# Performance work log

Hardware: AMD Instinct MI355X
Metric: run time of the kernel (lower is better)

The kernel has to match this reference:

```python
import jax, jax.numpy as jnp
import numpy as np

GAMMA = 0.7
WALK_LEN = 3
TAU = 1.0
N_FILTERS = 8


def _row_norm(A):
    return A / jnp.clip(jnp.sum(A, axis=-1, keepdims=True), 1e-12, None)


def _motif_channel(A, idx, Wadj, gates):
    # A: [n,n]; idx: [I,k] int node indices; Wadj: [F,k,k]; gates: [L]
    n = A.shape[0]
    I, k = idx.shape
    F = Wadj.shape[0]
    # learnable filter adjacency: softplus, symmetrize, zero diagonal, row-normalize
    S = jax.nn.softplus(Wadj)
    S = 0.5 * (S + jnp.swapaxes(S, -1, -2)) * (1.0 - jnp.eye(k, dtype=A.dtype))
    Sf = _row_norm(S)                                  # [F,k,k]
    # per-instance induced subgraph transition matrices
    As = A[idx[:, :, None], idx[:, None, :]]           # [I,k,k]
    Tm = _row_norm(As)                                 # [I,k,k]
    # batched Kronecker product: Km[i,f,a*k+b,c*k+d] = Tm[i,a,c]*Sf[f,b,d]
    Km = (Tm[:, None, :, None, :, None] * Sf[None, :, None, :, None, :]).reshape(I, F, k * k, k * k)
    gp = jax.nn.softplus(gates)                        # [L] length gates
    M = Km
    acc = (GAMMA * gp[0]) * jnp.trace(M, axis1=-2, axis2=-1)   # [I,F]
    for p in range(2, WALK_LEN + 1):
        M = M @ Km
        acc = acc + (GAMMA ** p * gp[p - 1]) * jnp.trace(M, axis1=-2, axis2=-1)
    sims = acc                                         # [I,F] RWK similarities
    alphas = jax.nn.softmax(sims / max(1e-06, TAU), axis=-1)
    contrib = (alphas * sims) / float(k)               # [I,F]
    upd = jnp.broadcast_to(contrib[:, None, :], (I, k, F)).reshape(I * k, F)
    return jnp.zeros((n, F), A.dtype).at[idx.reshape(-1)].add(upd)


def _layer(A, tri_idx, cyc_idx, H, Wt, Wc, g, lng, lnb, w1, b1, w2, b2):
    Phi = jnp.concatenate([_motif_channel(A, tri_idx, Wt, g),
                           _motif_channel(A, cyc_idx, Wc, g),
                           H], axis=1)                 # [n, in_ch]
    mu = jnp.mean(Phi, axis=-1, keepdims=True)
    var = jnp.var(Phi, axis=-1, keepdims=True)
    X = (Phi - mu) / jnp.sqrt(var + 1e-5) * lng + lnb  # LayerNorm
    return jax.nn.gelu(X @ w1 + b1, approximate=False) @ w2 + b2  # dropout = identity (eval)


def _templates():
    tri = np.zeros((3, 3), np.float32)
    for u, v in [(0, 1), (1, 2), (0, 2)]:
        tri[u, v] = tri[v, u] = 1.0
    cyc = np.zeros((4, 4), np.float32)
    for u, v in [(0, 1), (1, 2), (2, 3), (3, 0)]:
        cyc[u, v] = cyc[v, u] = 1.0
    return tri, cyc


def setup_inputs() -> dict:
    key = jax.random.key(0)
    ks = jax.random.split(key, 16)
    n, D, HID = 4096, 128, 128
    A = (jax.random.uniform(ks[0], (n, n)) < 0.01).astype(jnp.float32)
    A = 0.5 * (A + A.T)
    A = A * (1.0 - jnp.eye(n, dtype=jnp.float32))
    tri_idx = jax.random.randint(ks[1], (30000, 3), 0, n, dtype=jnp.int32)
    cyc_idx = jax.random.randint(ks[2], (15000, 4), 0, n, dtype=jnp.int32)
    tri_t, cyc_t = _templates()
    def w_adj(k, tmpl):
        return jnp.asarray(tmpl)[None] + 0.05 * jax.random.normal(k, (N_FILTERS,) + tmpl.shape, dtype=jnp.float32)
    in0, in1 = 17, 145
    inp = {"A_full": A, "tri_idx": tri_idx, "cyc_idx": cyc_idx,
           "W_tri_0": w_adj(ks[3], tri_t), "W_cyc_0": w_adj(ks[4], cyc_t),
           "gates_0": jnp.zeros((WALK_LEN,), jnp.float32),
           "lng_0": jnp.ones((in0,), jnp.float32), "lnb_0": jnp.zeros((in0,), jnp.float32),
           "w1_0": 0.05 * jax.random.normal(ks[5], (in0, HID), jnp.float32), "b1_0": jnp.zeros((HID,), jnp.float32),
           "w2_0": 0.05 * jax.random.normal(ks[6], (HID, D), jnp.float32), "b2_0": jnp.zeros((D,), jnp.float32),
           "W_tri_1": w_adj(ks[7], tri_t), "W_cyc_1": w_adj(ks[8], cyc_t),
           "gates_1": jnp.zeros((WALK_LEN,), jnp.float32),
           "lng_1": jnp.ones((in1,), jnp.float32), "lnb_1": jnp.zeros((in1,), jnp.float32),
           "w1_1": 0.05 * jax.random.normal(ks[9], (in1, HID), jnp.float32), "b1_1": jnp.zeros((HID,), jnp.float32),
           "w2_1": 0.05 * jax.random.normal(ks[10], (HID, D), jnp.float32), "b2_1": jnp.zeros((D,), jnp.float32)}
    return inp


def reference(A_full, tri_idx, cyc_idx,
              W_tri_0, W_cyc_0, gates_0, lng_0, lnb_0, w1_0, b1_0, w2_0, b2_0,
              W_tri_1, W_cyc_1, gates_1, lng_1, lnb_1, w1_1, b1_1, w2_1, b2_1):
    # base channel (use_base=True): node degree from dense adjacency
    H = jnp.sum(A_full, axis=-1, keepdims=True)        # [n,1]
    Z = _layer(A_full, tri_idx, cyc_idx, H, W_tri_0, W_cyc_0, gates_0, lng_0, lnb_0, w1_0, b1_0, w2_0, b2_0)
    H = jnp.concatenate([Z, H], axis=1)                # residual_cat: [n,129]
    Z = _layer(A_full, tri_idx, cyc_idx, H, W_tri_1, W_cyc_1, gates_1, lng_1, lnb_1, w1_1, b1_1, w2_1, b2_1)
    H = jnp.concatenate([Z, H], axis=1)                # [n,257]
    return H
```

## Files before the change

kernel.cpp:

```cpp
#include <hip/hip_runtime.h>
#include <math.h>
#include <stdint.h>

#define GAMMA 0.7f
#define QCAP 4608
#define NT 1024

typedef __attribute__((ext_vector_type(8))) short short8v;
typedef __attribute__((ext_vector_type(4))) float f32x4;

__device__ __forceinline__ float sp_dev(float x) {
    return fmaxf(x, 0.0f) + log1pf(expf(-fabsf(x)));
}
__device__ __forceinline__ float gelu_exact(float x) {
    return 0.5f * x * (1.0f + erff(x * 0.70710678118654752f));
}
__device__ __forceinline__ uint16_t f2bf(float x) {
    union { float f; uint32_t u; } c; c.f = x;
    uint32_t u = c.u + 0x7FFFu + ((c.u >> 16) & 1u);
    return (uint16_t)(u >> 16);
}

__device__ __forceinline__ short8v wfrag(const float* __restrict__ W, int col,
                                         int k0, int kmax) {
    short8v r;
#pragma unroll
    for (int j = 0; j < 8; j++) {
        int k = k0 + j;
        float v = (k < kmax) ? W[(size_t)k * 128 + col] : 0.0f;
        r[j] = (short)f2bf(v);
    }
    return r;
}

__global__ __launch_bounds__(NT) void uber_kernel(
    const float* __restrict__ A, const int* __restrict__ tri, const int* __restrict__ cyc,
    const float* __restrict__ Wt0, const float* __restrict__ Wc0, const float* __restrict__ g0,
    const float* __restrict__ lng0, const float* __restrict__ lnb0,
    const float* __restrict__ w1_0, const float* __restrict__ b1_0,
    const float* __restrict__ w2_0, const float* __restrict__ b2_0,
    const float* __restrict__ Wt1, const float* __restrict__ Wc1, const float* __restrict__ g1,
    const float* __restrict__ lng1, const float* __restrict__ lnb1,
    const float* __restrict__ w1_1, const float* __restrict__ b1_1,
    const float* __restrict__ w2_1, const float* __restrict__ b2_1,
    float* __restrict__ out, int n, int Itri, int Icyc) {

    __shared__ __align__(16) char upool[QCAP * 4];
    int* queue = (int*)upool;
    uint16_t (*Xs)[168] = (uint16_t(*)[168])upool;
    uint16_t (*Hs)[136] = (uint16_t(*)[136])(upool + 5376);
    float    (*Zs)[132] = (float(*)[132])(upool + 9728);
    __shared__ float dcs[2][2][8][3];
    __shared__ float phiL0[16][16];
    __shared__ float phiL1[16][16];
    __shared__ float h0s[16];
    __shared__ int qcnt;

    const int tid  = threadIdx.x;
    const int v0   = blockIdx.x * 16;
    const int wave = tid >> 6;
    const int lane = tid & 63;

    if (tid < 256) { ((float*)phiL0)[tid] = 0.0f; ((float*)phiL1)[tid] = 0.0f; }
    if (tid == 0) qcnt = 0;
    if (tid < 32) {
        int L = tid >> 4, m = (tid >> 3) & 1, f = tid & 7;
        int k = m ? 4 : 3;
        const float* W = L ? (m ? Wc1 : Wt1) : (m ? Wc0 : Wt0);
        const float* g = L ? g1 : g0;
        float S[4][4], Y[4][4];
        for (int a = 0; a < k; a++)
            for (int b = 0; b < k; b++)
                S[a][b] = sp_dev(W[(f * k + a) * k + b]);
        for (int a = 0; a < k; a++)
            for (int b = 0; b < k; b++)
                Y[a][b] = (a == b) ? 0.0f : 0.5f * (S[a][b] + S[b][a]);
        for (int a = 0; a < k; a++) {
            float rs = 0.0f;
            for (int b = 0; b < k; b++) rs += Y[a][b];
            rs = fmaxf(rs, 1e-12f);
            for (int b = 0; b < k; b++) Y[a][b] /= rs;
        }
        float t1 = 0, t2 = 0, t3 = 0;
        for (int a = 0; a < k; a++) t1 += Y[a][a];
        for (int a = 0; a < k; a++)
            for (int b = 0; b < k; b++) t2 += Y[a][b] * Y[b][a];
        for (int a = 0; a < k; a++)
            for (int b = 0; b < k; b++)
                for (int c = 0; c < k; c++) t3 += Y[a][b] * Y[b][c] * Y[c][a];
        dcs[m][L][f][0] = GAMMA * sp_dev(g[0]) * t1;
        dcs[m][L][f][1] = GAMMA * GAMMA * sp_dev(g[1]) * t2;
        dcs[m][L][f][2] = GAMMA * GAMMA * GAMMA * sp_dev(g[2]) * t3;
    }

    {
        int rr = wave;
        const float4* Ar = (const float4*)(A + (size_t)(v0 + rr) * n);
        int n4 = n >> 2;
        float s0 = 0, s1 = 0, s2 = 0, s3 = 0;
        for (int i = lane; i < n4; i += 256) {
            float4 a = Ar[i], b = Ar[i + 64], c = Ar[i + 128], d = Ar[i + 192];
            s0 += a.x + a.y + a.z + a.w;
            s1 += b.x + b.y + b.z + b.w;
            s2 += c.x + c.y + c.z + c.w;
            s3 += d.x + d.y + d.z + d.w;
        }
        float s = (s0 + s1) + (s2 + s3);
        for (int o = 32; o > 0; o >>= 1) s += __shfl_down(s, o);
        if (lane == 0) {
            h0s[rr] = s;
            out[(size_t)(v0 + rr) * 257 + 256] = s;
        }
    }
    __syncthreads();

    {
        int tot = Itri + Icyc;
        for (int base = 0; base < tot; base += NT) {
            int inst = base + tid;
            if (inst >= tot) break;
            int hit = 0;
            if (inst < Itri) {
                const int* p = tri + inst * 3;
#pragma unroll
                for (int j = 0; j < 3; j++) hit |= ((unsigned)(p[j] - v0) < 16u);
            } else {
                const int* p = cyc + (size_t)(inst - Itri) * 4;
#pragma unroll
                for (int j = 0; j < 4; j++) hit |= ((unsigned)(p[j] - v0) < 16u);
            }
            if (hit) {
                int q = atomicAdd(&qcnt, 1);
                if (q < QCAP) queue[q] = inst;
            }
        }
    }
    __syncthreads();

    {
        int qn = qcnt < QCAP ? qcnt : QCAP;
        for (int qi = tid; qi < qn; qi += NT) {
            int inst = queue[qi];
            bool isTri = inst < Itri;
            int m = isTri ? 0 : 1;
            float kinv = isTri ? (1.0f / 3.0f) : 0.25f;
            int nd[4];
            if (isTri) {
                const int* p = tri + inst * 3;
                nd[0] = p[0]; nd[1] = p[1]; nd[2] = p[2]; nd[3] = 0;
            } else {
                const int* p = cyc + (size_t)(inst - Itri) * 4;
                nd[0] = p[0]; nd[1] = p[1]; nd[2] = p[2]; nd[3] = p[3];
            }
            float M[4][4];
#pragma unroll
            for (int a = 0; a < 4; a++) {
                float rs = 0.0f;
#pragma unroll
                for (int b = 0; b < 4; b++) {
                    float v;
                    if (isTri)
                        v = (a < 3 && b < 3) ? A[(size_t)nd[a] * n + nd[b]]
                                             : ((a == 3 && b == 3) ? 1.0f : 0.0f);
                    else
                        v = A[(size_t)nd[a] * n + nd[b]];
                    M[a][b] = v; rs += v;
                }
                rs = fmaxf(rs, 1e-12f);
                float inv = 1.0f / rs;
#pragma unroll
                for (int b = 0; b < 4; b++) M[a][b] *= inv;
            }
            float t1 = M[0][0] + M[1][1] + M[2][2] + M[3][3];
            float t2 = 0, t3 = 0;
#pragma unroll
            for (int a = 0; a < 4; a++)
#pragma unroll
                for (int b = 0; b < 4; b++) {
                    float ab = M[a][b];
                    t2 += ab * M[b][a];
                    float a3 = 0;
#pragma unroll
                    for (int c = 0; c < 4; c++) a3 += M[b][c] * M[c][a];
                    t3 += ab * a3;
                }
            if (isTri) { t1 -= 1.0f; t2 -= 1.0f; t3 -= 1.0f; }

            float cn[2][8];
#pragma unroll
            for (int L = 0; L < 2; L++) {
                float sims[8], mx = -1e30f;
#pragma unroll
                for (int f = 0; f < 8; f++) {
                    sims[f] = dcs[m][L][f][0] * t1 + dcs[m][L][f][1] * t2 +
                              dcs[m][L][f][2] * t3;
                    mx = fmaxf(mx, sims[f]);
                }
                float se = 0;
#pragma unroll
                for (int f = 0; f < 8; f++) { float e = expf(sims[f] - mx); cn[L][f] = e; se += e; }
                float si = 1.0f / se;
#pragma unroll
                for (int f = 0; f < 8; f++) cn[L][f] = cn[L][f] * si * sims[f] * kinv;
            }
            int K = isTri ? 3 : 4;
#pragma unroll
            for (int j = 0; j < 4; j++) {
                if (j >= K) break;
                int r = nd[j] - v0;
                if ((unsigned)r < 16u) {
#pragma unroll
                    for (int f = 0; f < 8; f++) {
                        atomicAdd(&phiL0[r][m * 8 + f], cn[0][f]);
                        atomicAdd(&phiL1[r][m * 8 + f], cn[1][f]);
                    }
                }
            }
        }
    }
    __syncthreads();

    if (tid < 512) {
        int r = tid >> 5;
        int j = tid & 31;
        float x = (j < 16) ? phiL0[r][j] : (j == 16 ? h0s[r] : 0.0f);
        float s1 = x, s2 = x * x;
        for (int o = 16; o > 0; o >>= 1) { s1 += __shfl_xor(s1, o); s2 += __shfl_xor(s2, o); }
        float mu = s1 / 17.0f;
        float rstd = rsqrtf(s2 / 17.0f - mu * mu + 1e-5f);
        Xs[r][j] = (j < 17) ? f2bf((x - mu) * rstd * lng0[j] + lnb0[j]) : (uint16_t)0;
    }
    __syncthreads();

    if (tid < 512) {
        int w8 = tid >> 6, lr = lane & 15, lg = lane >> 4;
        int col = w8 * 16 + lr;
        f32x4 acc = {0.f, 0.f, 0.f, 0.f};
        short8v a = *(const short8v*)&Xs[lr][lg * 8];
        short8v b = wfrag(w1_0, col, lg * 8, 17);
        acc = __builtin_amdgcn_mfma_f32_16x16x32_bf16(a, b, acc, 0, 0, 0);
        float bias = b1_0[col];
#pragma unroll
        for (int i = 0; i < 4; i++)
            Hs[lg * 4 + i][col] = f2bf(gelu_exact(acc[i] + bias));
    }
    __syncthreads();

    if (tid < 512) {
        int w8 = tid >> 6, lr = lane & 15, lg = lane >> 4;
        int col = w8 * 16 + lr;
        f32x4 acc = {0.f, 0.f, 0.f, 0.f};
#pragma unroll
        for (int ks = 0; ks < 4; ks++) {
            short8v a = *(const short8v*)&Hs[lr][ks * 32 + lg * 8];
            short8v b = wfrag(w2_0, col, ks * 32 + lg * 8, 128);
            acc = __builtin_amdgcn_mfma_f32_16x16x32_bf16(a, b, acc, 0, 0, 0);
        }
        float bias = b2_0[col];
#pragma unroll
        for (int i = 0; i < 4; i++) {
            int row = lg * 4 + i;
            float val = acc[i] + bias;
            out[(size_t)(v0 + row) * 257 + 128 + col] = val;
            Zs[row][col] = val;
        }
    }
    __syncthreads();

    if (tid < 512) {
        int rr = tid >> 5;
        int t = tid & 31;
        float ph[5];
        float s1 = 0.0f, s2 = 0.0f;
#pragma unroll
        for (int s = 0; s < 5; s++) {
            int j = t + 32 * s;
            float x = 0.0f;
            if (j < 16) x = phiL1[rr][j];
            else if (j < 144) x = Zs[rr][j - 16];
            else if (j == 144) x = h0s[rr];
            ph[s] = x;
            if (j < 145) { s1 += x; s2 += x * x; }
        }
        for (int o = 16; o > 0; o >>= 1) { s1 += __shfl_xor(s1, o); s2 += __shfl_xor(s2, o); }
        float mu = s1 / 145.0f;
        float rstd = rsqrtf(s2 / 145.0f - mu * mu + 1e-5f);
#pragma unroll
        for (int s = 0; s < 5; s++) {
            int j = t + 32 * s;
            Xs[rr][j] = (j < 145) ? f2bf((ph[s] - mu) * rstd * lng1[j] + lnb1[j])
                                  : (uint16_t)0;
        }
    }
    __syncthreads();

    if (tid < 512) {
        int w8 = tid >> 6, lr = lane & 15, lg = lane >> 4;
        int col = w8 * 16 + lr;
        f32x4 acc = {0.f, 0.f, 0.f, 0.f};
#pragma unroll
        for (int ks = 0; ks < 5; ks++) {
            short8v a = *(const short8v*)&Xs[lr][ks * 32 + lg * 8];
            short8v b = wfrag(w1_1, col, ks * 32 + lg * 8, 145);
            acc = __builtin_amdgcn_mfma_f32_16x16x32_bf16(a, b, acc, 0, 0, 0);
        }
        float bias = b1_1[col];
#pragma unroll
        for (int i = 0; i < 4; i++)
            Hs[lg * 4 + i][col] = f2bf(gelu_exact(acc[i] + bias));
    }
    __syncthreads();

    if (tid < 512) {
        int w8 = tid >> 6, lr = lane & 15, lg = lane >> 4;
        int col = w8 * 16 + lr;
        f32x4 acc = {0.f, 0.f, 0.f, 0.f};
#pragma unroll
        for (int ks = 0; ks < 4; ks++) {
            short8v a = *(const short8v*)&Hs[lr][ks * 32 + lg * 8];
            short8v b = wfrag(w2_1, col, ks * 32 + lg * 8, 128);
            acc = __builtin_amdgcn_mfma_f32_16x16x32_bf16(a, b, acc, 0, 0, 0);
        }
        float bias = b2_1[col];
#pragma unroll
        for (int i = 0; i < 4; i++) {
            int row = lg * 4 + i;
            out[(size_t)(v0 + row) * 257 + col] = acc[i] + bias;
        }
    }
}

extern "C" void kernel_launch(void* const* d_in, const int* in_sizes, int n_in,
                              void* d_out, int out_size, void* d_ws, size_t ws_size,
                              hipStream_t stream) {
    const float* A    = (const float*)d_in[0];
    const int*   tri  = (const int*)d_in[1];
    const int*   cyc  = (const int*)d_in[2];

    int n    = out_size / 257;
    int Itri = in_sizes[1] / 3;
    int Icyc = in_sizes[2] / 4;

    uber_kernel<<<n / 16, NT, 0, stream>>>(
        A, tri, cyc,
        (const float*)d_in[3], (const float*)d_in[4], (const float*)d_in[5],
        (const float*)d_in[6], (const float*)d_in[7],
        (const float*)d_in[8], (const float*)d_in[9],
        (const float*)d_in[10], (const float*)d_in[11],
        (const float*)d_in[12], (const float*)d_in[13], (const float*)d_in[14],
        (const float*)d_in[15], (const float*)d_in[16],
        (const float*)d_in[17], (const float*)d_in[18],
        (const float*)d_in[19], (const float*)d_in[20],
        (float*)d_out, n, Itri, Icyc);
}
```

Measured before the change: 90.93 us.

## Split fused kernel into per-instance motif pass and per-node MLP pass

Adds a first kernel that computes each motif instance's softmax-weighted contribution exactly once, together with degree row sums and pre-packed bf16 transposed weight matrices written to workspace. The second kernel then only scans and scatters those precomputed contributions and loads the packed weight fragments directly. Previously each 16-node block recomputed the induced-subgraph traces for every instance it touched and converted fp32 weights to bf16 inline. The split removes that redundant per-block work but adds a second launch and workspace round trips, and the smaller QCAP could overflow on denser graphs.

```diff
diff --git a/kernel.cpp b/kernel.cpp
--- a/kernel.cpp
+++ b/kernel.cpp
@@ -3,8 +3,7 @@
 #include <stdint.h>
 
 #define GAMMA 0.7f
-#define QCAP 4608
-#define NT 1024
+#define QCAP 2048
 
 typedef __attribute__((ext_vector_type(8))) short short8v;
 typedef __attribute__((ext_vector_type(4))) float f32x4;
@@ -21,199 +20,235 @@
     return (uint16_t)(u >> 16);
 }
 
-__device__ __forceinline__ short8v wfrag(const float* __restrict__ W, int col,
-                                         int k0, int kmax) {
-    short8v r;
-#pragma unroll
-    for (int j = 0; j < 8; j++) {
-        int k = k0 + j;
-        float v = (k < kmax) ? W[(size_t)k * 128 + col] : 0.0f;
-        r[j] = (short)f2bf(v);
-    }
-    return r;
-}
-
-__global__ __launch_bounds__(NT) void uber_kernel(
+__global__ __launch_bounds__(256) void k1_kernel(
     const float* __restrict__ A, const int* __restrict__ tri, const int* __restrict__ cyc,
     const float* __restrict__ Wt0, const float* __restrict__ Wc0, const float* __restrict__ g0,
+    const float* __restrict__ Wt1, const float* __restrict__ Wc1, const float* __restrict__ g1,
+    const float* __restrict__ w1_0, const float* __restrict__ w2_0,
+    const float* __restrict__ w1_1, const float* __restrict__ w2_1,
+    float* __restrict__ cont, float* __restrict__ H0,
+    uint16_t* __restrict__ Wb10, uint16_t* __restrict__ Wb20,
+    uint16_t* __restrict__ Wb11, uint16_t* __restrict__ Wb21,
+    float* __restrict__ out, int n, int Itri, int Icyc, int BC) {
+
+    const int tid = threadIdx.x;
+    const int bid = blockIdx.x;
+    const int Itot = Itri + Icyc;
+
+    if (bid < BC) {
+        __shared__ float dcs[2][2][8][3];
+        if (tid < 32) {
+            int L = tid >> 4, m = (tid >> 3) & 1, f = tid & 7;
+            int k = m ? 4 : 3;
+            const float* W = L ? (m ? Wc1 : Wt1) : (m ? Wc0 : Wt0);
+            const float* g = L ? g1 : g0;
+            float S[4][4], Y[4][4];
+            for (int a = 0; a < k; a++)
+                for (int b = 0; b < k; b++)
+                    S[a][b] = sp_dev(W[(f * k + a) * k + b]);
+            for (int a = 0; a < k; a++)
+                for (int b = 0; b < k; b++)
+                    Y[a][b] = (a == b) ? 0.0f : 0.5f * (S[a][b] + S[b][a]);
+            for (int a = 0; a < k; a++) {
+                float rs = 0.0f;
+                for (int b = 0; b < k; b++) rs += Y[a][b];
+                rs = fmaxf(rs, 1e-12f);
+                for (int b = 0; b < k; b++) Y[a][b] /= rs;
+            }
+            float t1 = 0, t2 = 0, t3 = 0;
+            for (int a = 0; a < k; a++) t1 += Y[a][a];
+            for (int a = 0; a < k; a++)
+                for (int b = 0; b < k; b++) t2 += Y[a][b] * Y[b][a];
+            for (int a = 0; a < k; a++)
+                for (int b = 0; b < k; b++)
+                    for (int c = 0; c < k; c++) t3 += Y[a][b] * Y[b][c] * Y[c][a];
+            dcs[m][L][f][0] = GAMMA * sp_dev(g[0]) * t1;
+            dcs[m][L][f][1] = GAMMA * GAMMA * sp_dev(g[1]) * t2;
+            dcs[m][L][f][2] = GAMMA * GAMMA * GAMMA * sp_dev(g[2]) * t3;
+        }
+        __syncthreads();
+
+        int inst = bid * 256 + tid;
+        if (inst >= Itot) return;
+        bool isTri = inst < Itri;
+        int m = isTri ? 0 : 1;
+        float kinv = isTri ? (1.0f / 3.0f) : 0.25f;
+        int nd[4];
+        if (isTri) {
+            const int* p = tri + inst * 3;
+            nd[0] = p[0]; nd[1] = p[1]; nd[2] = p[2]; nd[3] = 0;
+        } else {
+            const int* p = cyc + (size_t)(inst - Itri) * 4;
+            nd[0] = p[0]; nd[1] = p[1]; nd[2] = p[2]; nd[3] = p[3];
+        }
+        float M[4][4];
+#pragma unroll
+        for (int a = 0; a < 4; a++) {
+            float rs = 0.0f;
+#pragma unroll
+            for (int b = 0; b < 4; b++) {
+                float v;
+                if (isTri)
+                    v = (a < 3 && b < 3) ? A[(size_t)nd[a] * n + nd[b]]
+                                         : ((a == 3 && b == 3) ? 1.0f : 0.0f);
+                else
+                    v = A[(size_t)nd[a] * n + nd[b]];
+                M[a][b] = v; rs += v;
+            }
+            rs = fmaxf(rs, 1e-12f);
+            float inv = 1.0f / rs;
+#pragma unroll
+            for (int b = 0; b < 4; b++) M[a][b] *= inv;
+        }
+        float t1 = M[0][0] + M[1][1] + M[2][2] + M[3][3];
+        float t2 = 0, t3 = 0;
+#pragma unroll
+        for (int a = 0; a < 4; a++)
+#pragma unroll
+            for (int b = 0; b < 4; b++) {
+                float ab = M[a][b];
+                t2 += ab * M[b][a];
+                float a3 = 0;
+#pragma unroll
+                for (int c = 0; c < 4; c++) a3 += M[b][c] * M[c][a];
+                t3 += ab * a3;
+            }
+        if (isTri) { t1 -= 1.0f; t2 -= 1.0f; t3 -= 1.0f; }
+
+#pragma unroll
+        for (int L = 0; L < 2; L++) {
+            float sims[8], mx = -1e30f;
+#pragma unroll
+            for (int f = 0; f < 8; f++) {
+                sims[f] = dcs[m][L][f][0] * t1 + dcs[m][L][f][1] * t2 +
+                          dcs[m][L][f][2] * t3;
+                mx = fmaxf(mx, sims[f]);
+            }
+            float es[8], se = 0;
+#pragma unroll
+            for (int f = 0; f < 8; f++) { es[f] = expf(sims[f] - mx); se += es[f]; }
+            float si = 1.0f / se;
+            f32x4 c0, c1;
+#pragma unroll
+            for (int f = 0; f < 4; f++) c0[f] = es[f] * si * sims[f] * kinv;
+#pragma unroll
+            for (int f = 0; f < 4; f++) c1[f] = es[f + 4] * si * sims[f + 4] * kinv;
+            float* cp = cont + ((size_t)L * Itot + inst) * 8;
+            *(f32x4*)cp = c0;
+            *(f32x4*)(cp + 4) = c1;
+        }
+    } else if (bid < BC + n) {
+        __shared__ float red[4];
+        int row = bid - BC;
+        const float4* Arow = (const float4*)(A + (size_t)row * n);
+        int n4 = n >> 2;
+        float s = 0.0f;
+        for (int i = tid; i < n4; i += 256) {
+            float4 v = Arow[i];
+            s += v.x + v.y + v.z + v.w;
+        }
+        for (int off = 32; off > 0; off >>= 1) s += __shfl_down(s, off);
+        if ((tid & 63) == 0) red[tid >> 6] = s;
+        __syncthreads();
+        if (tid == 0) {
+            float t = red[0] + red[1] + red[2] + red[3];
+            H0[row] = t;
+            out[(size_t)row * 257 + 256] = t;
+        }
+    } else {
+        int base = (bid - BC - n) * 4096;
+        for (int k = 0; k < 16; k++) {
+            int idx = base + k * 256 + tid;
+            if (idx >= 57344) break;
+            if (idx < 4096) {
+                int c = idx >> 5, kk = idx & 31;
+                Wb10[idx] = (kk < 17) ? f2bf(w1_0[kk * 128 + c]) : 0;
+            } else if (idx < 20480) {
+                int e = idx - 4096; int c = e >> 7, kk = e & 127;
+                Wb20[e] = f2bf(w2_0[kk * 128 + c]);
+            } else if (idx < 40960) {
+                int e = idx - 20480; int c = e / 160, kk = e % 160;
+                Wb11[e] = (kk < 145) ? f2bf(w1_1[kk * 128 + c]) : 0;
+            } else {
+                int e = idx - 40960; int c = e >> 7, kk = e & 127;
+                Wb21[e] = f2bf(w2_1[kk * 128 + c]);
+            }
+        }
+    }
+}
+
+__global__ __launch_bounds__(1024) void k2_kernel(
+    const int* __restrict__ tri, const int* __restrict__ cyc,
+    const float* __restrict__ cont, const float* __restrict__ H0,
     const float* __restrict__ lng0, const float* __restrict__ lnb0,
-    const float* __restrict__ w1_0, const float* __restrict__ b1_0,
-    const float* __restrict__ w2_0, const float* __restrict__ b2_0,
-    const float* __restrict__ Wt1, const float* __restrict__ Wc1, const float* __restrict__ g1,
+    const uint16_t* __restrict__ Wb10, const float* __restrict__ b1_0,
+    const uint16_t* __restrict__ Wb20, const float* __restrict__ b2_0,
     const float* __restrict__ lng1, const float* __restrict__ lnb1,
-    const float* __restrict__ w1_1, const float* __restrict__ b1_1,
-    const float* __restrict__ w2_1, const float* __restrict__ b2_1,
+    const uint16_t* __restrict__ Wb11, const float* __restrict__ b1_1,
+    const uint16_t* __restrict__ Wb21, const float* __restrict__ b2_1,
     float* __restrict__ out, int n, int Itri, int Icyc) {
 
-    __shared__ __align__(16) char upool[QCAP * 4];
+    __shared__ __align__(16) char upool[18432];
     int* queue = (int*)upool;
     uint16_t (*Xs)[168] = (uint16_t(*)[168])upool;
     uint16_t (*Hs)[136] = (uint16_t(*)[136])(upool + 5376);
     float    (*Zs)[132] = (float(*)[132])(upool + 9728);
-    __shared__ float dcs[2][2][8][3];
-    __shared__ float phiL0[16][16];
-    __shared__ float phiL1[16][16];
+    __shared__ float phi[2][16][16];
     __shared__ float h0s[16];
     __shared__ int qcnt;
 
     const int tid  = threadIdx.x;
     const int v0   = blockIdx.x * 16;
-    const int wave = tid >> 6;
     const int lane = tid & 63;
-
-    if (tid < 256) { ((float*)phiL0)[tid] = 0.0f; ((float*)phiL1)[tid] = 0.0f; }
+    const int Itot = Itri + Icyc;
+
+    if (tid < 512) ((float*)phi)[tid] = 0.0f;
     if (tid == 0) qcnt = 0;
-    if (tid < 32) {
-        int L = tid >> 4, m = (tid >> 3) & 1, f = tid & 7;
-        int k = m ? 4 : 3;
-        const float* W = L ? (m ? Wc1 : Wt1) : (m ? Wc0 : Wt0);
-        const float* g = L ? g1 : g0;
-        float S[4][4], Y[4][4];
-        for (int a = 0; a < k; a++)
-            for (int b = 0; b < k; b++)
-                S[a][b] = sp_dev(W[(f * k + a) * k + b]);
-        for (int a = 0; a < k; a++)
-            for (int b = 0; b < k; b++)
-                Y[a][b] = (a == b) ? 0.0f : 0.5f * (S[a][b] + S[b][a]);
-        for (int a = 0; a < k; a++) {
-            float rs = 0.0f;
-            for (int b = 0; b < k; b++) rs += Y[a][b];
-            rs = fmaxf(rs, 1e-12f);
-            for (int b = 0; b < k; b++) Y[a][b] /= rs;
-        }
-        float t1 = 0, t2 = 0, t3 = 0;
-        for (int a = 0; a < k; a++) t1 += Y[a][a];
-        for (int a = 0; a < k; a++)
-            for (int b = 0; b < k; b++) t2 += Y[a][b] * Y[b][a];
-        for (int a = 0; a < k; a++)
-            for (int b = 0; b < k; b++)
-                for (int c = 0; c < k; c++) t3 += Y[a][b] * Y[b][c] * Y[c][a];
-        dcs[m][L][f][0] = GAMMA * sp_dev(g[0]) * t1;
-        dcs[m][L][f][1] = GAMMA * GAMMA * sp_dev(g[1]) * t2;
-        dcs[m][L][f][2] = GAMMA * GAMMA * GAMMA * sp_dev(g[2]) * t3;
-    }
-
-    {
-        int rr = wave;
-        const float4* Ar = (const float4*)(A + (size_t)(v0 + rr) * n);
-        int n4 = n >> 2;
-        float s0 = 0, s1 = 0, s2 = 0, s3 = 0;
-        for (int i = lane; i < n4; i += 256) {
-            float4 a = Ar[i], b = Ar[i + 64], c = Ar[i + 128], d = Ar[i + 192];
-            s0 += a.x + a.y + a.z + a.w;
-            s1 += b.x + b.y + b.z + b.w;
-            s2 += c.x + c.y + c.z + c.w;
-            s3 += d.x + d.y + d.z + d.w;
-        }
-        float s = (s0 + s1) + (s2 + s3);
-        for (int o = 32; o > 0; o >>= 1) s += __shfl_down(s, o);
-        if (lane == 0) {
-            h0s[rr] = s;
-            out[(size_t)(v0 + rr) * 257 + 256] = s;
-        }
-    }
-    __syncthreads();
-
-    {
-        int tot = Itri + Icyc;
-        for (int base = 0; base < tot; base += NT) {
-            int inst = base + tid;
-            if (inst >= tot) break;
-            int hit = 0;
-            if (inst < Itri) {
-                const int* p = tri + inst * 3;
-#pragma unroll
-                for (int j = 0; j < 3; j++) hit |= ((unsigned)(p[j] - v0) < 16u);
-            } else {
-                const int* p = cyc + (size_t)(inst - Itri) * 4;
-#pragma unroll
-                for (int j = 0; j < 4; j++) hit |= ((unsigned)(p[j] - v0) < 16u);
-            }
-            if (hit) {
-                int q = atomicAdd(&qcnt, 1);
-                if (q < QCAP) queue[q] = inst;
-            }
+    if (tid >= 512 && tid < 528) h0s[tid - 512] = H0[v0 + (tid - 512)];
+    __syncthreads();
+
+    for (int base = 0; base < Itot; base += 1024) {
+        int inst = base + tid;
+        if (inst >= Itot) break;
+        int hit = 0;
+        if (inst < Itri) {
+            const int* p = tri + inst * 3;
+#pragma unroll
+            for (int j = 0; j < 3; j++) hit |= ((unsigned)(p[j] - v0) < 16u);
+        } else {
+            const int* p = cyc + (size_t)(inst - Itri) * 4;
+#pragma unroll
+            for (int j = 0; j < 4; j++) hit |= ((unsigned)(p[j] - v0) < 16u);
+        }
+        if (hit) {
+            int q = atomicAdd(&qcnt, 1);
+            if (q < QCAP) queue[q] = inst;
         }
     }
     __syncthreads();
 
     {
         int qn = qcnt < QCAP ? qcnt : QCAP;
-        for (int qi = tid; qi < qn; qi += NT) {
+        for (int it = tid; it < 2 * qn; it += 1024) {
+            int qi = it >> 1, L = it & 1;
             int inst = queue[qi];
             bool isTri = inst < Itri;
+            int K = isTri ? 3 : 4;
             int m = isTri ? 0 : 1;
-            float kinv = isTri ? (1.0f / 3.0f) : 0.25f;
-            int nd[4];
-            if (isTri) {
-                const int* p = tri + inst * 3;
-                nd[0] = p[0]; nd[1] = p[1]; nd[2] = p[2]; nd[3] = 0;
-            } else {
-                const int* p = cyc + (size_t)(inst - Itri) * 4;
-                nd[0] = p[0]; nd[1] = p[1]; nd[2] = p[2]; nd[3] = p[3];
-            }
-            float M[4][4];
-#pragma unroll
-            for (int a = 0; a < 4; a++) {
-                float rs = 0.0f;
-#pragma unroll
-                for (int b = 0; b < 4; b++) {
-                    float v;
-                    if (isTri)
-                        v = (a < 3 && b < 3) ? A[(size_t)nd[a] * n + nd[b]]
-                                             : ((a == 3 && b == 3) ? 1.0f : 0.0f);
-                    else
-                        v = A[(size_t)nd[a] * n + nd[b]];
-                    M[a][b] = v; rs += v;
-                }
-                rs = fmaxf(rs, 1e-12f);
-                float inv = 1.0f / rs;
-#pragma unroll
-                for (int b = 0; b < 4; b++) M[a][b] *= inv;
-            }
-            float t1 = M[0][0] + M[1][1] + M[2][2] + M[3][3];
-            float t2 = 0, t3 = 0;
-#pragma unroll
-            for (int a = 0; a < 4; a++)
-#pragma unroll
-                for (int b = 0; b < 4; b++) {
-                    float ab = M[a][b];
-                    t2 += ab * M[b][a];
-                    float a3 = 0;
-#pragma unroll
-                    for (int c = 0; c < 4; c++) a3 += M[b][c] * M[c][a];
-                    t3 += ab * a3;
-                }
-            if (isTri) { t1 -= 1.0f; t2 -= 1.0f; t3 -= 1.0f; }
-
-            float cn[2][8];
-#pragma unroll
-            for (int L = 0; L < 2; L++) {
-                float sims[8], mx = -1e30f;
-#pragma unroll
-                for (int f = 0; f < 8; f++) {
-                    sims[f] = dcs[m][L][f][0] * t1 + dcs[m][L][f][1] * t2 +
-                              dcs[m][L][f][2] * t3;
-                    mx = fmaxf(mx, sims[f]);
-                }
-                float se = 0;
-#pragma unroll
-                for (int f = 0; f < 8; f++) { float e = expf(sims[f] - mx); cn[L][f] = e; se += e; }
-                float si = 1.0f / se;
-#pragma unroll
-                for (int f = 0; f < 8; f++) cn[L][f] = cn[L][f] * si * sims[f] * kinv;
-            }
-            int K = isTri ? 3 : 4;
+            const int* p = isTri ? tri + inst * 3 : cyc + (size_t)(inst - Itri) * 4;
+            const float* cp = cont + ((size_t)L * Itot + inst) * 8;
+            float4 c0 = *(const float4*)cp;
+            float4 c1 = *(const float4*)(cp + 4);
 #pragma unroll
             for (int j = 0; j < 4; j++) {
                 if (j >= K) break;
-                int r = nd[j] - v0;
+                int r = p[j] - v0;
                 if ((unsigned)r < 16u) {
-#pragma unroll
-                    for (int f = 0; f < 8; f++) {
-                        atomicAdd(&phiL0[r][m * 8 + f], cn[0][f]);
-                        atomicAdd(&phiL1[r][m * 8 + f], cn[1][f]);
-                    }
+                    float* dst = &phi[L][r][m * 8];
+                    atomicAdd(&dst[0], c0.x); atomicAdd(&dst[1], c0.y);
+                    atomicAdd(&dst[2], c0.z); atomicAdd(&dst[3], c0.w);
+                    atomicAdd(&dst[4], c1.x); atomicAdd(&dst[5], c1.y);
+                    atomicAdd(&dst[6], c1.z); atomicAdd(&dst[7], c1.w);
                 }
             }
         }
@@ -223,7 +258,7 @@
     if (tid < 512) {
         int r = tid >> 5;
         int j = tid & 31;
-        float x = (j < 16) ? phiL0[r][j] : (j == 16 ? h0s[r] : 0.0f);
+        float x = (j < 16) ? phi[0][r][j] : (j == 16 ? h0s[r] : 0.0f);
         float s1 = x, s2 = x * x;
         for (int o = 16; o > 0; o >>= 1) { s1 += __shfl_xor(s1, o); s2 += __shfl_xor(s2, o); }
         float mu = s1 / 17.0f;
@@ -237,7 +272,7 @@
         int col = w8 * 16 + lr;
         f32x4 acc = {0.f, 0.f, 0.f, 0.f};
         short8v a = *(const short8v*)&Xs[lr][lg * 8];
-        short8v b = wfrag(w1_0, col, lg * 8, 17);
+        short8v b = *(const short8v*)(Wb10 + (size_t)col * 32 + lg * 8);
         acc = __builtin_amdgcn_mfma_f32_16x16x32_bf16(a, b, acc, 0, 0, 0);
         float bias = b1_0[col];
 #pragma unroll
@@ -253,7 +288,7 @@
 #pragma unroll
         for (int ks = 0; ks < 4; ks++) {
             short8v a = *(const short8v*)&Hs[lr][ks * 32 + lg * 8];
-            short8v b = wfrag(w2_0, col, ks * 32 + lg * 8, 128);
+            short8v b = *(const short8v*)(Wb20 + (size_t)col * 128 + ks * 32 + lg * 8);
             acc = __builtin_amdgcn_mfma_f32_16x16x32_bf16(a, b, acc, 0, 0, 0);
         }
         float bias = b2_0[col];
@@ -276,7 +311,7 @@
         for (int s = 0; s < 5; s++) {
             int j = t + 32 * s;
             float x = 0.0f;
-            if (j < 16) x = phiL1[rr][j];
+            if (j < 16) x = phi[1][rr][j];
             else if (j < 144) x = Zs[rr][j - 16];
             else if (j == 144) x = h0s[rr];
             ph[s] = x;
@@ -301,7 +336,7 @@
 #pragma unroll
         for (int ks = 0; ks < 5; ks++) {
             short8v a = *(const short8v*)&Xs[lr][ks * 32 + lg * 8];
-            short8v b = wfrag(w1_1, col, ks * 32 + lg * 8, 145);
+            short8v b = *(const short8v*)(Wb11 + (size_t)col * 160 + ks * 32 + lg * 8);
             acc = __builtin_amdgcn_mfma_f32_16x16x32_bf16(a, b, acc, 0, 0, 0);
         }
         float bias = b1_1[col];
@@ -318,7 +353,7 @@
 #pragma unroll
         for (int ks = 0; ks < 4; ks++) {
             short8v a = *(const short8v*)&Hs[lr][ks * 32 + lg * 8];
-            short8v b = wfrag(w2_1, col, ks * 32 + lg * 8, 128);
+            short8v b = *(const short8v*)(Wb21 + (size_t)col * 128 + ks * 32 + lg * 8);
             acc = __builtin_amdgcn_mfma_f32_16x16x32_bf16(a, b, acc, 0, 0, 0);
         }
         float bias = b2_1[col];
@@ -340,16 +375,32 @@
     int n    = out_size / 257;
     int Itri = in_sizes[1] / 3;
     int Icyc = in_sizes[2] / 4;
-
-    uber_kernel<<<n / 16, NT, 0, stream>>>(
+    int Itot = Itri + Icyc;
+
+    float* ws = (float*)d_ws;
+    float* H0   = ws;
+    float* cont = ws + n;
+    uint16_t* Wb10 = (uint16_t*)(cont + (size_t)2 * Itot * 8);
+    uint16_t* Wb20 = Wb10 + 128 * 32;
+    uint16_t* Wb11 = Wb20 + 128 * 128;
+    uint16_t* Wb21 = Wb11 + 128 * 160;
+    float* out = (float*)d_out;
+
+    int BC = (Itot + 255) / 256;
+    int BP = 14;
+    k1_kernel<<<BC + n + BP, 256, 0, stream>>>(
         A, tri, cyc,
         (const float*)d_in[3], (const float*)d_in[4], (const float*)d_in[5],
+        (const float*)d_in[12], (const float*)d_in[13], (const float*)d_in[14],
+        (const float*)d_in[8], (const float*)d_in[10],
+        (const float*)d_in[17], (const float*)d_in[19],
+        cont, H0, Wb10, Wb20, Wb11, Wb21, out, n, Itri, Icyc, BC);
+
+    k2_kernel<<<n / 16, 1024, 0, stream>>>(
+        tri, cyc, cont, H0,
         (const float*)d_in[6], (const float*)d_in[7],
-        (const float*)d_in[8], (const float*)d_in[9],
-        (const float*)d_in[10], (const float*)d_in[11],
-        (const float*)d_in[12], (const float*)d_in[13], (const float*)d_in[14],
+        Wb10, (const float*)d_in[9], Wb20, (const float*)d_in[11],
         (const float*)d_in[15], (const float*)d_in[16],
-        (const float*)d_in[17], (const float*)d_in[18],
-        (const float*)d_in[19], (const float*)d_in[20],
-        (float*)d_out, n, Itri, Icyc);
-}
+        Wb11, (const float*)d_in[18], Wb21, (const float*)d_in[20],
+        out, n, Itri, Icyc);
+}
```

After: 99.33 us. +9.2%, slower.
